# Performance work log

Hardware: AMD Instinct MI355X
Metric: run time of the kernel (lower is better)

## Reference

```python
import jax, jax.numpy as jnp
import numpy as np

D_MODEL = 1024
N_HEADS = 16
HEAD_DIM = D_MODEL // N_HEADS  # 64
BATCH, SEQ = 2, 2048
MASK_FILL = -1000000000.0


def setup_inputs() -> dict:
    key = jax.random.key(0)
    ks = jax.random.split(key, 13)
    s = 1.0 / np.sqrt(D_MODEL)
    inp = {
        "q": jax.random.normal(ks[0], (BATCH, SEQ, D_MODEL), jnp.float32),
        "k": jax.random.normal(ks[1], (BATCH, SEQ, D_MODEL), jnp.float32),
        "v": jax.random.normal(ks[2], (BATCH, SEQ, D_MODEL), jnp.float32),
        "mask": jax.random.randint(ks[3], (BATCH, 1, SEQ, SEQ), 0, 2, jnp.int32),
        "Wq": jax.random.normal(ks[4], (D_MODEL, D_MODEL), jnp.float32) * s,
        "bq": jax.random.normal(ks[5], (D_MODEL,), jnp.float32) * s,
        "Wk": jax.random.normal(ks[6], (D_MODEL, D_MODEL), jnp.float32) * s,
        "bk": jax.random.normal(ks[7], (D_MODEL,), jnp.float32) * s,
        "Wv": jax.random.normal(ks[8], (D_MODEL, D_MODEL), jnp.float32) * s,
        "bv": jax.random.normal(ks[9], (D_MODEL,), jnp.float32) * s,
        "Wo": jax.random.normal(ks[10], (D_MODEL, D_MODEL), jnp.float32) * s,
        "bo": jax.random.normal(ks[11], (D_MODEL,), jnp.float32) * s,
    }
    return inp


def reference(q, k, v, mask, Wq, bq, Wk, bk, Wv, bv, Wo, bo):
    batch, seq, feat = q.shape
    # Linear projections (torch Linear: x @ W.T + b)
    qp = q @ Wq.T + bq
    kp = k @ Wk.T + bk
    vp = v @ Wv.T + bv

    def split(x):
        # (B, S, D) -> (B, H, S, Dh)
        return x.reshape(batch, seq, N_HEADS, HEAD_DIM).swapaxes(1, 2)

    qh, kh, vh = split(qp), split(kp), split(vp)

    # (B, H, S, S) score matrix, scaled
    score = jnp.einsum("bhqd,bhkd->bhqk", qh, kh) / jnp.sqrt(
        jnp.asarray(HEAD_DIM, qh.dtype))
    score = jnp.where(mask == 0, jnp.asarray(MASK_FILL, score.dtype), score)
    attn = jax.nn.softmax(score, axis=-1)
    out = jnp.einsum("bhqk,bhkd->bhqd", attn, vh)  # (B, H, S, Dh)
    joint = out.swapaxes(1, 2).reshape(batch, seq, feat)
    return joint @ Wo.T + bo
```

## Files before the change

### kernel.cpp

```cpp
#include <hip/hip_runtime.h>

typedef unsigned short u16;
typedef unsigned long long u64;
typedef float f32x4 __attribute__((ext_vector_type(4)));
typedef __bf16 bf16x8 __attribute__((ext_vector_type(8)));
typedef u16 u16x8 __attribute__((ext_vector_type(8)));
typedef u16 u16x4 __attribute__((ext_vector_type(4)));

#define QSCALE 0.18033688011112042f

__device__ __forceinline__ u16 f2bf(float f) {
  unsigned int u = __float_as_uint(f);
  u += 0x7fffu + ((u >> 16) & 1u);
  return (u16)(u >> 16);
}

__device__ __forceinline__ void async16(const void* g, void* l) {
  __builtin_amdgcn_global_load_lds(
      (__attribute__((address_space(1))) void*)g,
      (__attribute__((address_space(3))) void*)l,
      16, 0, 0);
}

__device__ __forceinline__ f32x4 mfma16(bf16x8 a, bf16x8 b, f32x4 c) {
  return __builtin_amdgcn_mfma_f32_16x16x32_bf16(a, b, c, 0, 0, 0);
}

struct CvtArgs {
  const float* src[7];
  u16* dst[7];
};

__global__ __launch_bounds__(256) void cvt_kernel(CvtArgs a) {
  int z = blockIdx.z;
  int n = (z < 3) ? 4194304 : 1048576;
  int base = (blockIdx.x * 256 + threadIdx.x) * 8;
  if (base >= n) return;
  const float* s = a.src[z] + base;
  f32x4 x0 = *(const f32x4*)s;
  f32x4 x1 = *(const f32x4*)(s + 4);
  u16x8 pk;
  pk[0]=f2bf(x0[0]); pk[1]=f2bf(x0[1]); pk[2]=f2bf(x0[2]); pk[3]=f2bf(x0[3]);
  pk[4]=f2bf(x1[0]); pk[5]=f2bf(x1[1]); pk[6]=f2bf(x1[2]); pk[7]=f2bf(x1[3]);
  *(u16x8*)(a.dst[z] + base) = pk;
}

__global__ __launch_bounds__(256) void pack_mask_kernel(
    const int* __restrict__ mask, u64* __restrict__ pm) {
  int idx = blockIdx.x * 256 + threadIdx.x;
  const int4* src = (const int4*)(mask + (size_t)idx * 64);
  u64 bits = 0ull;
#pragma unroll
  for (int j = 0; j < 16; ++j) {
    int4 v = src[j];
    if (v.x) bits |= 1ull << (4 * j + 0);
    if (v.y) bits |= 1ull << (4 * j + 1);
    if (v.z) bits |= 1ull << (4 * j + 2);
    if (v.w) bits |= 1ull << (4 * j + 3);
  }
  pm[idx] = bits;
}

__device__ __forceinline__ void gemm_body(const u16* __restrict__ A,
                                          const u16* __restrict__ W,
                                          const float* __restrict__ bias,
                                          void* __restrict__ outraw, int mode,
                                          float oscale) {
  alignas(16) __shared__ u16 lA[128 * 32];
  alignas(16) __shared__ u16 lB[128 * 32];
  const int tid = threadIdx.x;
  const int lane = tid & 63, wv = tid >> 6;
  const int wm = wv >> 1, wn = wv & 1;
  const int m0 = blockIdx.y * 128, n0 = blockIdx.x * 128;
  const int l15 = lane & 15, quad = lane >> 4;
  const int srow = lane >> 2;
  const int scol = (lane & 3) * 8;

  f32x4 acc[4][4] = {};

  for (int k0 = 0; k0 < 1024; k0 += 32) {
#pragma unroll
    for (int t = 0; t < 2; ++t) {
      int rb = (wv * 2 + t) * 16;
      async16(A + (size_t)(m0 + rb + srow) * 1024 + k0 + scol, (char*)lA + rb * 64);
      async16(W + (size_t)(n0 + rb + srow) * 1024 + k0 + scol, (char*)lB + rb * 64);
    }
    __syncthreads();
    bf16x8 af[4], bfr[4];
#pragma unroll
    for (int i = 0; i < 4; ++i) {
      af[i]  = *(const bf16x8*)(lA + (wm * 64 + i * 16 + l15) * 32 + quad * 8);
      bfr[i] = *(const bf16x8*)(lB + (wn * 64 + i * 16 + l15) * 32 + quad * 8);
    }
#pragma unroll
    for (int i = 0; i < 4; ++i)
#pragma unroll
      for (int j = 0; j < 4; ++j)
        acc[i][j] = mfma16(af[i], bfr[j], acc[i][j]);
    __syncthreads();
  }

#pragma unroll
  for (int i = 0; i < 4; ++i) {
    int mbase = m0 + wm * 64 + i * 16 + quad * 4;
#pragma unroll
    for (int j = 0; j < 4; ++j) {
      int n = n0 + wn * 64 + j * 16 + l15;
      float bv = bias[n];
#pragma unroll
      for (int r = 0; r < 4; ++r) {
        int m = mbase + r;
        float val = (acc[i][j][r] + bv) * oscale;
        if (mode == 0) {
          int b = m >> 11, s = m & 2047, h = n >> 6, dh = n & 63;
          ((u16*)outraw)[((((size_t)b * 16 + h) * 2048 + s) << 6) + dh] = f2bf(val);
        } else if (mode == 1) {
          int b = m >> 11, s = m & 2047, h = n >> 6, dh = n & 63;
          ((u16*)outraw)[((((size_t)b * 16 + h) * 64 + dh) << 11) + s] = f2bf(val);
        } else {
          ((float*)outraw)[(size_t)m * 1024 + n] = val;
        }
      }
    }
  }
}

__global__ __launch_bounds__(256) void gemm_qkv_kernel(
    const u16* __restrict__ qb, const u16* __restrict__ kb, const u16* __restrict__ vb,
    const u16* __restrict__ Wqb, const float* __restrict__ bq,
    const u16* __restrict__ Wkb, const float* __restrict__ bk,
    const u16* __restrict__ Wvb, const float* __restrict__ bv,
    u16* __restrict__ qp, u16* __restrict__ kp, u16* __restrict__ vt) {
  if (blockIdx.z == 0)      gemm_body(qb, Wqb, bq, qp, 0, QSCALE);
  else if (blockIdx.z == 1) gemm_body(kb, Wkb, bk, kp, 0, 1.0f);
  else                      gemm_body(vb, Wvb, bv, vt, 1, 1.0f);
}

__global__ __launch_bounds__(256) void gemm_o_kernel(
    const u16* __restrict__ joint, const u16* __restrict__ Wob,
    const float* __restrict__ bo, float* __restrict__ out) {
  gemm_body(joint, Wob, bo, out, 2, 1.0f);
}

__global__ __launch_bounds__(256) void attn_kernel(
    const u16* __restrict__ qp, const u16* __restrict__ kp,
    const u16* __restrict__ vt, const u64* __restrict__ pm,
    u16* __restrict__ joint) {
  alignas(16) __shared__ u16 kbuf[2][4096];
  alignas(16) __shared__ u16 vbuf[2][4096];
  alignas(16) __shared__ u16 pbuf[4][1024];

  const int tid = threadIdx.x, lane = tid & 63, wv = tid >> 6;
  const int quad = lane >> 4, l15 = lane & 15;
  const int q0 = blockIdx.x * 64;
  const int h = blockIdx.y, b = blockIdx.z;
  const size_t head_off = ((size_t)b * 16 + h) * 2048 * 64;
  const u16* Qh = qp + head_off;
  const u16* Kh = kp + head_off;
  const u16* Vh = vt + head_off;
  const int q = q0 + wv * 16 + l15;
  const u64* pmq = pm + ((size_t)b * 2048 + q) * 32;
  u16* pslice = pbuf[wv];

  bf16x8 qf0, qf1;
  {
    const u16* qrow = Qh + (size_t)q * 64 + quad * 8;
    qf0 = *(const bf16x8*)(qrow);
    qf1 = *(const bf16x8*)(qrow + 32);
  }


  f32x4 O[4] = {};
  float l_part = 0.f;

#pragma unroll
  for (int i = 0; i < 2; ++i) {
    int d = i * 256 + tid;
    int nt = d >> 7, half = (d >> 6) & 1, l6 = d & 63;
    async16(Kh + (size_t)(nt * 16 + (l6 & 15)) * 64 + half * 32 + (l6 >> 4) * 8,
            (char*)kbuf[0] + d * 16);
    int blk = d >> 6;
    async16(Vh + (size_t)((blk >> 1) * 16 + (l6 & 15)) * 2048 + (blk & 1) * 32 + (l6 >> 4) * 8,
            (char*)vbuf[0] + d * 16);
  }

  for (int kt = 0; kt < 32; ++kt) {
    __syncthreads();

    if (kt != 31) {
      const int nb = (kt + 1) * 64;
      u16* kd = kbuf[(kt + 1) & 1];
      u16* vd = vbuf[(kt + 1) & 1];
#pragma unroll
      for (int i = 0; i < 2; ++i) {
        int d = i * 256 + tid;
        int nt = d >> 7, half = (d >> 6) & 1, l6 = d & 63;
        async16(Kh + (size_t)(nb + nt * 16 + (l6 & 15)) * 64 + half * 32 + (l6 >> 4) * 8,
                (char*)kd + d * 16);
        int blk = d >> 6;
        async16(Vh + (size_t)((blk >> 1) * 16 + (l6 & 15)) * 2048 + nb + (blk & 1) * 32 + (l6 >> 4) * 8,
                (char*)vd + d * 16);
      }
    }

    const u16* kc = kbuf[kt & 1];
    const u16* vc = vbuf[kt & 1];
    u64 word = pmq[kt];

    f32x4 S[4];
#pragma unroll
    for (int nt = 0; nt < 4; ++nt) {
      bf16x8 kf0 = *(const bf16x8*)(kc + nt * 1024 + lane * 8);
      bf16x8 kf1 = *(const bf16x8*)(kc + nt * 1024 + 512 + lane * 8);
      f32x4 z = {};
      z = mfma16(kf0, qf0, z);
      S[nt] = mfma16(kf1, qf1, z);
    }

    unsigned int wlo = (unsigned int)word, whi = (unsigned int)(word >> 32);
#pragma unroll
    for (int nt = 0; nt < 4; ++nt) {
      unsigned int hw = (nt < 2) ? wlo : whi;
      unsigned int nib = hw >> ((nt & 1) * 16 + quad * 4);
#pragma unroll
      for (int r = 0; r < 4; ++r) {
        float pe = __builtin_amdgcn_exp2f(S[nt][r]);
        float p = ((nib >> r) & 1u) ? pe : 0.f;
        S[nt][r] = p;
        l_part += p;
      }
    }

#pragma unroll
    for (int nt = 0; nt < 4; ++nt) {
      unsigned int lo = (unsigned int)f2bf(S[nt][0]) | ((unsigned int)f2bf(S[nt][1]) << 16);
      unsigned int hi = (unsigned int)f2bf(S[nt][2]) | ((unsigned int)f2bf(S[nt][3]) << 16);
      int t4 = 4 * nt + quad;
      int ks = t4 >> 3;
      int qd = (t4 & 7) >> 1;
      u16* pw = pslice + ks * 512 + qd * 128 + l15 * 8 + (t4 & 1) * 4;
      *(u64*)pw = (u64)lo | ((u64)hi << 32);
    }
    asm volatile("s_waitcnt lgkmcnt(0)" ::: "memory");

#pragma unroll
    for (int ks = 0; ks < 2; ++ks) {
      bf16x8 pf = *(const bf16x8*)(pslice + ks * 512 + lane * 8);
#pragma unroll
      for (int nt = 0; nt < 4; ++nt) {
        bf16x8 vf = *(const bf16x8*)(vc + (nt * 2 + ks) * 512 + lane * 8);
        O[nt] = mfma16(vf, pf, O[nt]);
      }
    }
  }

  float l = l_part;
  l += __shfl_xor(l, 16, 64);
  l += __shfl_xor(l, 32, 64);
  float inv = 1.0f / l;
  size_t row_off = ((size_t)b * 2048 + q) * 1024 + h * 64;
#pragma unroll
  for (int nt = 0; nt < 4; ++nt) {
    u16x4 ov;
#pragma unroll
    for (int r = 0; r < 4; ++r) ov[r] = f2bf(O[nt][r] * inv);
    *(u16x4*)(joint + row_off + nt * 16 + quad * 4) = ov;
  }
}

extern "C" void kernel_launch(void* const* d_in, const int* in_sizes, int n_in,
                              void* d_out, int out_size, void* d_ws, size_t ws_size,
                              hipStream_t stream) {
  const float* q  = (const float*)d_in[0];
  const float* k  = (const float*)d_in[1];
  const float* v  = (const float*)d_in[2];
  const int* mask = (const int*)d_in[3];
  const float* Wq = (const float*)d_in[4];
  const float* bq = (const float*)d_in[5];
  const float* Wk = (const float*)d_in[6];
  const float* bk = (const float*)d_in[7];
  const float* Wv = (const float*)d_in[8];
  const float* bv = (const float*)d_in[9];
  const float* Wo = (const float*)d_in[10];
  const float* bo = (const float*)d_in[11];
  float* out = (float*)d_out;

  u16* w = (u16*)d_ws;
  u16* qp    = w;
  u16* kp    = w + 4194304;
  u16* vt    = w + 8388608;
  u16* qb    = w + 12582912;
  u16* kb    = w + 16777216;
  u16* vb    = w + 20971520;
  u16* Wqb   = w + 25165824;
  u16* Wkb   = w + 26214400;
  u16* Wvb   = w + 27262976;
  u16* Wob   = w + 28311552;
  u64* pm    = (u64*)(w + 29360128);
  u16* joint = qb;

  CvtArgs ca;
  ca.src[0] = q;  ca.dst[0] = qb;
  ca.src[1] = k;  ca.dst[1] = kb;
  ca.src[2] = v;  ca.dst[2] = vb;
  ca.src[3] = Wq; ca.dst[3] = Wqb;
  ca.src[4] = Wk; ca.dst[4] = Wkb;
  ca.src[5] = Wv; ca.dst[5] = Wvb;
  ca.src[6] = Wo; ca.dst[6] = Wob;

  pack_mask_kernel<<<dim3(512), dim3(256), 0, stream>>>(mask, pm);
  cvt_kernel<<<dim3(2048, 1, 7), dim3(256), 0, stream>>>(ca);
  gemm_qkv_kernel<<<dim3(8, 32, 3), dim3(256), 0, stream>>>(
      qb, kb, vb, Wqb, bq, Wkb, bk, Wvb, bv, qp, kp, vt);
  attn_kernel<<<dim3(32, 16, 2), dim3(256), 0, stream>>>(qp, kp, vt, pm, joint);
  gemm_o_kernel<<<dim3(8, 32, 1), dim3(256), 0, stream>>>(joint, Wob, bo, out);
}
```

Measured before the change: 301.4 us.

## Load V fragments directly from global to registers, drop V LDS staging

The attention kernel no longer stages V tiles through shared memory. Each lane loads its V MFMA fragments straight from global memory into registers at the start of each key tile. This halves the LDS footprint and async copy traffic, and adds a launch-bounds occupancy hint of 4 blocks. It also swaps manual float-to-bf16 rounding for vector convert builtins. The risk is that the direct global loads are issued right before use with no prefetch, which may expose memory latency. Every query block also re-reads V without sharing it across waves.

Measured after the change: 381.8 us. 26.7% more time.

```diff
diff --git a/kernel.cpp b/kernel.cpp
--- a/kernel.cpp
+++ b/kernel.cpp
@@ -3,6 +3,7 @@
 typedef unsigned short u16;
 typedef unsigned long long u64;
 typedef float f32x4 __attribute__((ext_vector_type(4)));
+typedef __bf16 bf16x4 __attribute__((ext_vector_type(4)));
 typedef __bf16 bf16x8 __attribute__((ext_vector_type(8)));
 typedef u16 u16x8 __attribute__((ext_vector_type(8)));
 typedef u16 u16x4 __attribute__((ext_vector_type(4)));
@@ -142,12 +143,11 @@
   gemm_body(joint, Wob, bo, out, 2, 1.0f);
 }
 
-__global__ __launch_bounds__(256) void attn_kernel(
+__global__ __launch_bounds__(256, 4) void attn_kernel(
     const u16* __restrict__ qp, const u16* __restrict__ kp,
     const u16* __restrict__ vt, const u64* __restrict__ pm,
     u16* __restrict__ joint) {
   alignas(16) __shared__ u16 kbuf[2][4096];
-  alignas(16) __shared__ u16 vbuf[2][4096];
   alignas(16) __shared__ u16 pbuf[4][1024];
 
   const int tid = threadIdx.x, lane = tid & 63, wv = tid >> 6;
@@ -169,42 +169,39 @@
     qf1 = *(const bf16x8*)(qrow + 32);
   }
 
+  const u16* vbase = Vh + (size_t)l15 * 2048 + quad * 8;
+
+  const int sd0 = tid, sd1 = 256 + tid;
+  const int snt0 = sd0 >> 7, shalf0 = (sd0 >> 6) & 1, sl60 = sd0 & 63;
+  const int snt1 = sd1 >> 7, shalf1 = (sd1 >> 6) & 1, sl61 = sd1 & 63;
+  const u16* kg0 = Kh + (size_t)(snt0 * 16 + (sl60 & 15)) * 64 + shalf0 * 32 + (sl60 >> 4) * 8;
+  const u16* kg1 = Kh + (size_t)(snt1 * 16 + (sl61 & 15)) * 64 + shalf1 * 32 + (sl61 >> 4) * 8;
 
   f32x4 O[4] = {};
   float l_part = 0.f;
 
-#pragma unroll
-  for (int i = 0; i < 2; ++i) {
-    int d = i * 256 + tid;
-    int nt = d >> 7, half = (d >> 6) & 1, l6 = d & 63;
-    async16(Kh + (size_t)(nt * 16 + (l6 & 15)) * 64 + half * 32 + (l6 >> 4) * 8,
-            (char*)kbuf[0] + d * 16);
-    int blk = d >> 6;
-    async16(Vh + (size_t)((blk >> 1) * 16 + (l6 & 15)) * 2048 + (blk & 1) * 32 + (l6 >> 4) * 8,
-            (char*)vbuf[0] + d * 16);
-  }
+  async16(kg0, (char*)kbuf[0] + sd0 * 16);
+  async16(kg1, (char*)kbuf[0] + sd1 * 16);
 
   for (int kt = 0; kt < 32; ++kt) {
     __syncthreads();
 
+    bf16x8 vfr[8];
+#pragma unroll
+    for (int nt = 0; nt < 4; ++nt)
+#pragma unroll
+      for (int ks = 0; ks < 2; ++ks)
+        vfr[nt * 2 + ks] =
+            *(const bf16x8*)(vbase + (size_t)nt * 32768 + kt * 64 + ks * 32);
+
     if (kt != 31) {
-      const int nb = (kt + 1) * 64;
-      u16* kd = kbuf[(kt + 1) & 1];
-      u16* vd = vbuf[(kt + 1) & 1];
-#pragma unroll
-      for (int i = 0; i < 2; ++i) {
-        int d = i * 256 + tid;
-        int nt = d >> 7, half = (d >> 6) & 1, l6 = d & 63;
-        async16(Kh + (size_t)(nb + nt * 16 + (l6 & 15)) * 64 + half * 32 + (l6 >> 4) * 8,
-                (char*)kd + d * 16);
-        int blk = d >> 6;
-        async16(Vh + (size_t)((blk >> 1) * 16 + (l6 & 15)) * 2048 + nb + (blk & 1) * 32 + (l6 >> 4) * 8,
-                (char*)vd + d * 16);
-      }
+      const size_t adv = (size_t)(kt + 1) * 64 * 64;
+      char* kd = (char*)kbuf[(kt + 1) & 1];
+      async16(kg0 + adv, kd + sd0 * 16);
+      async16(kg1 + adv, kd + sd1 * 16);
     }
 
     const u16* kc = kbuf[kt & 1];
-    const u16* vc = vbuf[kt & 1];
     u64 word = pmq[kt];
 
     f32x4 S[4];
@@ -233,13 +230,12 @@
 
 #pragma unroll
     for (int nt = 0; nt < 4; ++nt) {
-      unsigned int lo = (unsigned int)f2bf(S[nt][0]) | ((unsigned int)f2bf(S[nt][1]) << 16);
-      unsigned int hi = (unsigned int)f2bf(S[nt][2]) | ((unsigned int)f2bf(S[nt][3]) << 16);
+      bf16x4 pv = __builtin_convertvector(S[nt], bf16x4);
       int t4 = 4 * nt + quad;
       int ks = t4 >> 3;
       int qd = (t4 & 7) >> 1;
       u16* pw = pslice + ks * 512 + qd * 128 + l15 * 8 + (t4 & 1) * 4;
-      *(u64*)pw = (u64)lo | ((u64)hi << 32);
+      *(u64*)pw = *(const u64*)&pv;
     }
     asm volatile("s_waitcnt lgkmcnt(0)" ::: "memory");
 
@@ -247,10 +243,8 @@
     for (int ks = 0; ks < 2; ++ks) {
       bf16x8 pf = *(const bf16x8*)(pslice + ks * 512 + lane * 8);
 #pragma unroll
-      for (int nt = 0; nt < 4; ++nt) {
-        bf16x8 vf = *(const bf16x8*)(vc + (nt * 2 + ks) * 512 + lane * 8);
-        O[nt] = mfma16(vf, pf, O[nt]);
-      }
+      for (int nt = 0; nt < 4; ++nt)
+        O[nt] = mfma16(vfr[nt * 2 + ks], pf, O[nt]);
     }
   }
 
@@ -261,10 +255,9 @@
   size_t row_off = ((size_t)b * 2048 + q) * 1024 + h * 64;
 #pragma unroll
   for (int nt = 0; nt < 4; ++nt) {
-    u16x4 ov;
-#pragma unroll
-    for (int r = 0; r < 4; ++r) ov[r] = f2bf(O[nt][r] * inv);
-    *(u16x4*)(joint + row_off + nt * 16 + quad * 4) = ov;
+    f32x4 ov = O[nt] * inv;
+    bf16x4 obv = __builtin_convertvector(ov, bf16x4);
+    *(u64*)(joint + row_off + nt * 16 + quad * 4) = *(const u64*)&obv;
   }
 }
 
```
